# Kernel tuning notes

Hardware: AMD Instinct MI355X
Metric: run time of the kernel (lower is better)

## Reference

```python
import jax, jax.numpy as jnp
import numpy as np
from jax import lax

SEQ_LEN = 8192
NUM_LABELS = 512


def setup_inputs() -> dict:
    key = jax.random.key(0)
    k1, k2 = jax.random.split(key)
    feats = jax.random.normal(k1, (SEQ_LEN, NUM_LABELS), dtype=jnp.float32)
    # nn.Parameter(torch.randn(L, L))
    transitions = jax.random.normal(k2, (NUM_LABELS, NUM_LABELS), dtype=jnp.float32)
    return {"feats": feats, "transitions": transitions}


def reference(feats, transitions):
    """Viterbi decode, matching CRFLayer.forward.

    feats:       [T, L] emission scores
    transitions: [L, L], transitions[i, j] = score of i -> j
    Returns (viterbi_score [], viterbi_path [T] int32).
    """
    # Forward max-plus scan.  scores_with_transitions[i, j] = scores[i] + T[i, j];
    # max/argmax over source label i (dim 0), exactly as in _viterbi_decode.
    def step(scores, emis):
        m = scores[:, None] + transitions            # [L, L]
        bp = jnp.argmax(m, axis=0).astype(jnp.int32)  # [L]
        new_scores = emis + jnp.max(m, axis=0)        # [L]
        return new_scores, bp

    init = feats[0]  # scores = zeros + emissions[0]
    final_scores, back_pointers = lax.scan(step, init, feats[1:])  # bps: [T-1, L]

    last_tag = jnp.argmax(final_scores).astype(jnp.int32)
    viterbi_score = jnp.max(final_scores)

    # Backtrack: t_{T-1} = last_tag; t_i = back_pointers[i][t_{i+1}].
    def back(tag, bp):
        prev = bp[tag]
        return prev, prev

    _, path_prefix = lax.scan(back, last_tag, back_pointers, reverse=True)  # [T-1]
    viterbi_path = jnp.concatenate([path_prefix, last_tag[None]])           # [T]
    return viterbi_score, viterbi_path
```

## Files before the change

kernel.cpp:

```cpp
#include <hip/hip_runtime.h>
#include <cstdint>
#include <cstddef>

#define L 512
#define TSTEPS 8192
#define NSEG 64
#define SEGLEN (TSTEPS / NSEG)
#define WARM 32
#define CHUNK 128
#define NCHUNK 64

typedef float f4 __attribute__((ext_vector_type(4)));
typedef unsigned int u32;

static constexpr size_t OFF_SCORES = 0;
static constexpr size_t OFF_WARM   = (size_t)TSTEPS * L * 4;
static constexpr size_t OFF_BP     = OFF_WARM + (size_t)NSEG * WARM * L * 4;
static constexpr size_t OFF_EXIT   = OFF_BP + (size_t)TSTEPS * L * 2;
static constexpr size_t OFF_ENTRY  = OFF_EXIT + (size_t)NCHUNK * L * 2;
static constexpr size_t OFF_PATH   = OFF_ENTRY + NCHUNK * sizeof(int);

__device__ __forceinline__ void st_coh(float* p, float v) {
  __hip_atomic_store((u32*)p, __float_as_uint(v), __ATOMIC_RELAXED, __HIP_MEMORY_SCOPE_AGENT);
}
__device__ __forceinline__ u32 myumax(u32 a, u32 b) { return a > b ? a : b; }

#define UMX(V) myumax(myumax(__float_as_uint(V.x), __float_as_uint(V.y)), \
                      myumax(__float_as_uint(V.z), __float_as_uint(V.w)))

#define POLL2(P)                                                 \
  asm volatile(                                                  \
      "global_load_dwordx4 %0, %2, off sc0 sc1\n\t"              \
      "global_load_dwordx4 %1, %2, off offset:16 sc0 sc1\n\t"    \
      "s_waitcnt vmcnt(0)"                                       \
      : "=&v"(B0), "=&v"(B1) : "v"(P) : "memory")

__global__ __launch_bounds__(1024, 4) void scan_kernel(const float* __restrict__ feats,
                                                       const float* __restrict__ trans,
                                                       float* __restrict__ scores,
                                                       float* __restrict__ warm,
                                                       uint16_t* __restrict__ bp) {
  __shared__ float s_row[8 * 68];

  const int seg  = blockIdx.x >> 2;
  const int b    = blockIdx.x & 3;
  const int tid  = threadIdx.x;
  const int w    = tid >> 6;
  const int lane = tid & 63;
  const int sub  = lane & 7;
  const int cid  = lane >> 3;
  const int col0 = b * 128;
  const int col  = col0 + w * 8 + cid;
  const int rowbase = sub * 64;

  const int a     = seg * SEGLEN;
  const int start = (seg == 0) ? 0 : a - WARM;
  const int tend  = (seg == NSEG - 1) ? (TSTEPS - 1) : (a + SEGLEN - 1);

  auto rowptr = [&](int t) -> float* {
    return (t >= a - 1) ? scores + (size_t)t * L
                        : warm + ((size_t)seg * WARM + (t - start)) * L;
  };

  f4 Tr[16];
  #pragma unroll
  for (int q = 0; q < 16; ++q) {
    Tr[q].x = trans[(size_t)(rowbase + q * 4 + 0) * L + col];
    Tr[q].y = trans[(size_t)(rowbase + q * 4 + 1) * L + col];
    Tr[q].z = trans[(size_t)(rowbase + q * 4 + 2) * L + col];
    Tr[q].w = trans[(size_t)(rowbase + q * 4 + 3) * L + col];
  }

  if (tid < 128) st_coh(rowptr(start) + col0 + tid, feats[(size_t)start * L + col0 + tid]);

  for (int t = start + 1; t <= tend; ++t) {
    float e = 0.f;
    if (sub == 0) e = feats[(size_t)t * L + col];

    if (w == 15) {
      const float* p = rowptr(t - 1) + lane * 8;
      f4 B0, B1;
      int tries = 0;
      for (;;) {
        POLL2(p);
        if (!__any(myumax(UMX(B0), UMX(B1)) == 0xFFFFFFFFu)) break;
        if (++tries > 2) __builtin_amdgcn_s_sleep(1);
      }
      *(f4*)(s_row + (lane >> 3) * 68 + (lane & 7) * 8)     = B0;
      *(f4*)(s_row + (lane >> 3) * 68 + (lane & 7) * 8 + 4) = B1;
    }
    __syncthreads();

    float bv = -__builtin_inff(); int bi = 0;
    #pragma unroll
    for (int q = 0; q < 16; ++q) {
      f4 sv = *(const f4*)(s_row + sub * 68 + q * 4);
      float c0 = sv.x + Tr[q].x;
      float c1 = sv.y + Tr[q].y;
      float c2 = sv.z + Tr[q].z;
      float c3 = sv.w + Tr[q].w;
      if (c0 > bv) { bv = c0; bi = rowbase + q * 4 + 0; }
      if (c1 > bv) { bv = c1; bi = rowbase + q * 4 + 1; }
      if (c2 > bv) { bv = c2; bi = rowbase + q * 4 + 2; }
      if (c3 > bv) { bv = c3; bi = rowbase + q * 4 + 3; }
    }
    #pragma unroll
    for (int off = 1; off <= 4; off <<= 1) {
      float ov = __shfl_xor(bv, off);
      int   oi = __shfl_xor(bi, off);
      if (ov > bv || (ov == bv && oi < bi)) { bv = ov; bi = oi; }
    }
    if (sub == 0) {
      if (t <= a + SEGLEN - 2 || seg == NSEG - 1)
        st_coh(rowptr(t) + col, bv + e);
      if (t >= a)
        bp[(size_t)t * L + col] = (uint16_t)bi;
    }
  }
}

__global__ __launch_bounds__(512) void exitmap_kernel(const uint16_t* __restrict__ bp,
                                                      uint16_t* __restrict__ cexit) {
  extern __shared__ char smem[];
  uint16_t* bpl = (uint16_t*)smem;
  const int c = blockIdx.x, tid = threadIdx.x;
  const int lo = c * CHUNK;
  const int hi = min(lo + CHUNK, TSTEPS - 1);
  const int nrows = hi - lo;
  const u32* src = (const u32*)(bp + (size_t)(lo + 1) * L);
  u32* dst = (u32*)bpl;
  for (int idx = tid; idx < nrows * (L / 2); idx += 512) dst[idx] = src[idx];
  __syncthreads();
  int e = tid;
  for (int r = nrows - 1; r >= 0; --r) e = bpl[r * L + e];
  cexit[(size_t)c * L + tid] = (uint16_t)e;
}

__global__ __launch_bounds__(64) void compose_kernel(const float* __restrict__ scores,
                                                     const uint16_t* __restrict__ cexit,
                                                     int* __restrict__ entryTag,
                                                     int* __restrict__ pathbuf,
                                                     float* __restrict__ out) {
  const int lane = threadIdx.x;
  float bv = -__builtin_inff(); int bi = 0;
  #pragma unroll
  for (int r = 0; r < 8; ++r) {
    int i = r * 64 + lane;
    float v = scores[(size_t)(TSTEPS - 1) * L + i];
    if (v > bv) { bv = v; bi = i; }
  }
  #pragma unroll
  for (int off = 1; off < 64; off <<= 1) {
    float ov = __shfl_xor(bv, off);
    int   oi = __shfl_xor(bi, off);
    bool take = (ov > bv) || (ov == bv && oi < bi);
    bv = take ? ov : bv; bi = take ? oi : bi;
  }
  if (lane == 0) {
    out[1 + (TSTEPS - 1)] = (float)bi;
    pathbuf[TSTEPS - 1] = bi;
    int e = bi;
    entryTag[NCHUNK - 1] = e;
    for (int c = NCHUNK - 1; c >= 1; --c) {
      e = cexit[(size_t)c * L + e];
      entryTag[c - 1] = e;
    }
  }
}

__global__ __launch_bounds__(512) void extract_kernel(const uint16_t* __restrict__ bp,
                                                      const int* __restrict__ entryTag,
                                                      int* __restrict__ pathbuf,
                                                      float* __restrict__ out) {
  extern __shared__ char smem[];
  uint16_t* bpl = (uint16_t*)smem;
  const int c = blockIdx.x, tid = threadIdx.x;
  const int lo = c * CHUNK;
  const int hi = min(lo + CHUNK, TSTEPS - 1);
  const int nrows = hi - lo;
  const u32* src = (const u32*)(bp + (size_t)(lo + 1) * L);
  u32* dst = (u32*)bpl;
  for (int idx = tid; idx < nrows * (L / 2); idx += 512) dst[idx] = src[idx];
  __syncthreads();
  if (tid == 0) {
    int e = entryTag[c];
    for (int t = hi - 1; t >= lo; --t) {
      e = bpl[(t - lo) * L + e];
      out[1 + t] = (float)e;
      pathbuf[t] = e;
    }
  }
}

__global__ __launch_bounds__(512) void score_kernel(const float* __restrict__ feats,
                                                    const float* __restrict__ trans,
                                                    const int* __restrict__ pathbuf,
                                                    float* __restrict__ out) {
  __shared__ int pl[TSTEPS];
  __shared__ float red[512];
  const int tid = threadIdx.x;
  for (int i = tid; i < TSTEPS; i += 512) pl[i] = pathbuf[i];
  __syncthreads();
  float s = 0.f;
  #pragma unroll 4
  for (int k = 0; k < 16; ++k) {
    int t = tid * 16 + k;
    s += feats[(size_t)t * L + pl[t]];
    if (t < TSTEPS - 1) s += trans[(size_t)pl[t] * L + pl[t + 1]];
  }
  red[tid] = s;
  __syncthreads();
  for (int w = 256; w > 0; w >>= 1) {
    if (tid < w) red[tid] += red[tid + w];
    __syncthreads();
  }
  if (tid == 0) out[0] = red[0];
}

extern "C" void kernel_launch(void* const* d_in, const int* in_sizes, int n_in,
                              void* d_out, int out_size, void* d_ws, size_t ws_size,
                              hipStream_t stream) {
  const float* feats = (const float*)d_in[0];
  const float* trans = (const float*)d_in[1];
  float* out = (float*)d_out;
  char* ws = (char*)d_ws;
  float*    scores  = (float*)(ws + OFF_SCORES);
  float*    warm    = (float*)(ws + OFF_WARM);
  uint16_t* bp      = (uint16_t*)(ws + OFF_BP);
  uint16_t* cexit   = (uint16_t*)(ws + OFF_EXIT);
  int*      entry   = (int*)(ws + OFF_ENTRY);
  int*      pathbuf = (int*)(ws + OFF_PATH);

  const int CH_LDS = CHUNK * L * 2;

  hipFuncSetAttribute((const void*)exitmap_kernel, hipFuncAttributeMaxDynamicSharedMemorySize, CH_LDS);
  hipFuncSetAttribute((const void*)extract_kernel, hipFuncAttributeMaxDynamicSharedMemorySize, CH_LDS);

  hipMemsetAsync(scores, 0xFF, (size_t)(TSTEPS + NSEG * WARM) * L * sizeof(float), stream);

  scan_kernel<<<NSEG * 4, 1024, 0, stream>>>(feats, trans, scores, warm, bp);
  exitmap_kernel<<<NCHUNK, 512, CH_LDS, stream>>>(bp, cexit);
  compose_kernel<<<1, 64, 0, stream>>>(scores, cexit, entry, pathbuf, out);
  extract_kernel<<<NCHUNK, 512, CH_LDS, stream>>>(bp, entry, pathbuf, out);
  score_kernel<<<1, 512, 0, stream>>>(feats, trans, pathbuf, out);
}
```

Before: 527.6 us.

## Add fast-path L2-scoped polling with credit fallback and remap segment block order

Producers now write each score both with an sc0 store and an agent-scope coherent store. Consumers first poll with cheaper sc0-only loads for a few tries, tracked by a credit counter, before falling back to the system-coherent sc0 sc1 polling loop. The block-to-segment mapping is also changed so the four column blocks of a segment are spread across the grid instead of adjacent. This aims to cut cross-block handoff latency in the serial scan. It doubles the store traffic and relies on the cache-coherence behavior of sc0 loads across XCDs, which may be unsafe or slow.

Result: slower. 1.487 ms (+181.8%).

```diff
diff --git a/kernel.cpp b/kernel.cpp
--- a/kernel.cpp
+++ b/kernel.cpp
@@ -23,12 +23,22 @@
 __device__ __forceinline__ void st_coh(float* p, float v) {
   __hip_atomic_store((u32*)p, __float_as_uint(v), __ATOMIC_RELAXED, __HIP_MEMORY_SCOPE_AGENT);
 }
+__device__ __forceinline__ void st_fast(float* p, float v) {
+  asm volatile("global_store_dword %0, %1, off sc0" :: "v"(p), "v"(v) : "memory");
+}
 __device__ __forceinline__ u32 myumax(u32 a, u32 b) { return a > b ? a : b; }
 
 #define UMX(V) myumax(myumax(__float_as_uint(V.x), __float_as_uint(V.y)), \
                       myumax(__float_as_uint(V.z), __float_as_uint(V.w)))
 
-#define POLL2(P)                                                 \
+#define POLLF(P)                                                 \
+  asm volatile(                                                  \
+      "global_load_dwordx4 %0, %2, off sc0\n\t"                  \
+      "global_load_dwordx4 %1, %2, off offset:16 sc0\n\t"        \
+      "s_waitcnt vmcnt(0)"                                       \
+      : "=&v"(B0), "=&v"(B1) : "v"(P) : "memory")
+
+#define POLLS(P)                                                 \
   asm volatile(                                                  \
       "global_load_dwordx4 %0, %2, off sc0 sc1\n\t"              \
       "global_load_dwordx4 %1, %2, off offset:16 sc0 sc1\n\t"    \
@@ -42,8 +52,8 @@
                                                        uint16_t* __restrict__ bp) {
   __shared__ float s_row[8 * 68];
 
-  const int seg  = blockIdx.x >> 2;
-  const int b    = blockIdx.x & 3;
+  const int seg  = blockIdx.x & 63;
+  const int b    = blockIdx.x >> 6;
   const int tid  = threadIdx.x;
   const int w    = tid >> 6;
   const int lane = tid & 63;
@@ -71,7 +81,13 @@
     Tr[q].w = trans[(size_t)(rowbase + q * 4 + 3) * L + col];
   }
 
-  if (tid < 128) st_coh(rowptr(start) + col0 + tid, feats[(size_t)start * L + col0 + tid]);
+  if (tid < 128) {
+    float v = feats[(size_t)start * L + col0 + tid];
+    st_fast(rowptr(start) + col0 + tid, v);
+    st_coh(rowptr(start) + col0 + tid, v);
+  }
+
+  int credit = 16;
 
   for (int t = start + 1; t <= tend; ++t) {
     float e = 0.f;
@@ -80,11 +96,22 @@
     if (w == 15) {
       const float* p = rowptr(t - 1) + lane * 8;
       f4 B0, B1;
-      int tries = 0;
-      for (;;) {
-        POLL2(p);
-        if (!__any(myumax(UMX(B0), UMX(B1)) == 0xFFFFFFFFu)) break;
-        if (++tries > 2) __builtin_amdgcn_s_sleep(1);
+      bool got = false;
+      if (credit > 0) {
+        #pragma unroll 1
+        for (int it = 0; it < 3; ++it) {
+          POLLF(p);
+          if (!__any(myumax(UMX(B0), UMX(B1)) == 0xFFFFFFFFu)) { got = true; break; }
+        }
+        credit = got ? 16 : (credit - 1);
+      }
+      if (!got) {
+        int tries = 0;
+        for (;;) {
+          POLLS(p);
+          if (!__any(myumax(UMX(B0), UMX(B1)) == 0xFFFFFFFFu)) break;
+          if (++tries > 2) __builtin_amdgcn_s_sleep(1);
+        }
       }
       *(f4*)(s_row + (lane >> 3) * 68 + (lane & 7) * 8)     = B0;
       *(f4*)(s_row + (lane >> 3) * 68 + (lane & 7) * 8 + 4) = B1;
@@ -111,8 +138,11 @@
       if (ov > bv || (ov == bv && oi < bi)) { bv = ov; bi = oi; }
     }
     if (sub == 0) {
-      if (t <= a + SEGLEN - 2 || seg == NSEG - 1)
-        st_coh(rowptr(t) + col, bv + e);
+      if (t <= a + SEGLEN - 2 || seg == NSEG - 1) {
+        float* dst = rowptr(t) + col;
+        st_fast(dst, bv + e);
+        st_coh(dst, bv + e);
+      }
       if (t >= a)
         bp[(size_t)t * L + col] = (uint16_t)bi;
     }
```
